# Kernel tuning notes

Measured on AMD Instinct MI355X. Metric: run time of the kernel, lower is better.

## Reference

```python
import jax, jax.numpy as jnp
import numpy as np

B, S, D, H = 2, 2048, 768, 12
DK = D // H
DF = 3072
SOFTCAP = 30.0
LN_EPS = 1e-5
NEG_INF = -1e30


def layer_norm(x, g, b):
    m = jnp.mean(x, axis=-1, keepdims=True)
    v = jnp.mean(jnp.square(x - m), axis=-1, keepdims=True)
    return (x - m) * jax.lax.rsqrt(v + LN_EPS) * g + b


def setup_inputs() -> dict:
    key = jax.random.key(0)
    ks = jax.random.split(key, 12)
    s = 0.02
    x = jax.random.normal(ks[0], (B, S, D), jnp.float32)
    count_bias = jax.random.normal(ks[1], (B, 1, S, S), jnp.float32)
    # causal mask: True = allowed
    attn_mask = jnp.broadcast_to(jnp.tril(jnp.ones((S, S), bool)), (B, 1, S, S))
    Wq = jax.random.normal(ks[2], (D, D), jnp.float32) * s
    Wk = jax.random.normal(ks[3], (D, D), jnp.float32) * s
    Wv = jax.random.normal(ks[4], (D, D), jnp.float32) * s
    Wo = jax.random.normal(ks[5], (D, D), jnp.float32) * s
    W1 = jax.random.normal(ks[6], (D, DF), jnp.float32) * s
    W2 = jax.random.normal(ks[7], (DF, D), jnp.float32) * s
    g1 = jnp.ones((D,), jnp.float32)
    b1 = jnp.zeros((D,), jnp.float32)
    g2 = jnp.ones((D,), jnp.float32)
    b2 = jnp.zeros((D,), jnp.float32)
    return dict(x=x, count_bias=count_bias, attn_mask=attn_mask, Wq=Wq, Wk=Wk,
                Wv=Wv, Wo=Wo, W1=W1, W2=W2, g1=g1, b1=b1, g2=g2, b2=b2)


def reference(x, count_bias, attn_mask, Wq, Wk, Wv, Wo, W1, W2, g1, b1, g2, b2):
    # pre-norm (note: residual taken from normed activations, faithful to source)
    h = layer_norm(x, g1, b1)                                   # (B,S,D)
    q = (h @ Wq).reshape(B, S, H, DK).transpose(0, 2, 1, 3)     # (B,H,S,DK)
    k = (h @ Wk).reshape(B, S, H, DK).transpose(0, 2, 1, 3)
    v = (h @ Wv).reshape(B, S, H, DK).transpose(0, 2, 1, 3)
    scale = 1.0 / np.sqrt(DK).astype(np.float32)
    scores = jnp.einsum('bhqd,bhkd->bhqk', q, k) * scale + count_bias
    scores = jnp.tanh(scores / SOFTCAP) * SOFTCAP               # softcap
    scores = jnp.where(attn_mask, scores, NEG_INF)
    weights = jax.nn.softmax(scores, axis=-1)
    o = jnp.einsum('bhqk,bhkd->bhqd', weights, v)               # (B,H,S,DK)
    o = o.transpose(0, 2, 1, 3).reshape(B, S, D) @ Wo
    x1 = o + h
    h2 = layer_norm(x1, g2, b2)
    ffn = jax.nn.gelu(h2 @ W1, approximate=False) @ W2
    return ffn + h2
```

## Files before the change

### kernel.cpp

```cpp
#include <hip/hip_runtime.h>
#include <hip/hip_bf16.h>
#include <cstdint>

#define Bn 2
#define Sn 2048
#define Dn 768
#define Hn 12
#define DKn 64
#define DFn 3072
#define Mrows 4096

typedef float f32x4 __attribute__((ext_vector_type(4)));
typedef __bf16 bf16x8 __attribute__((ext_vector_type(8)));
typedef short s16x8 __attribute__((ext_vector_type(8)));
typedef short s16x4 __attribute__((ext_vector_type(4)));

__device__ __forceinline__ f32x4 MFMA(s16x8 a, s16x8 b, f32x4 c) {
  return __builtin_amdgcn_mfma_f32_16x16x32_bf16(
      __builtin_bit_cast(bf16x8, a), __builtin_bit_cast(bf16x8, b), c, 0, 0, 0);
}

__device__ __forceinline__ void g2lds16(const void* g, void* l) {
  __builtin_amdgcn_global_load_lds(
      (__attribute__((address_space(1))) void*)(g),
      (__attribute__((address_space(3))) void*)(l), 16, 0, 0);
}

__device__ __forceinline__ short f2bf(float f) {
  unsigned u = __builtin_bit_cast(unsigned, f);
  unsigned r = (u + 0x7fffu + ((u >> 16) & 1u)) >> 16;
  return (short)r;
}

__global__ void wtrans(const float* __restrict__ in, short* __restrict__ out, int R, int C) {
  __shared__ float t[32][33];
  int c0 = blockIdx.x * 32, r0 = blockIdx.y * 32;
  int tx = threadIdx.x, ty = threadIdx.y;
#pragma unroll
  for (int i = 0; i < 4; i++) t[ty + i * 8][tx] = in[(size_t)(r0 + ty + i * 8) * C + c0 + tx];
  __syncthreads();
#pragma unroll
  for (int i = 0; i < 4; i++) out[(size_t)(c0 + ty + i * 8) * R + r0 + tx] = f2bf(t[tx][ty + i * 8]);
}

__global__ __launch_bounds__(256) void ln_kernel(const float* __restrict__ x,
                                                 const float* __restrict__ g,
                                                 const float* __restrict__ b,
                                                 short* __restrict__ hb,
                                                 float* __restrict__ hf) {
  int row = blockIdx.x;
  const float* xr = x + (size_t)row * Dn;
  int tid = threadIdx.x;
  float v[3];
  float s = 0.f, ss = 0.f;
#pragma unroll
  for (int i = 0; i < 3; i++) {
    v[i] = xr[tid + i * 256];
    s += v[i];
    ss += v[i] * v[i];
  }
#pragma unroll
  for (int m = 1; m < 64; m <<= 1) {
    s += __shfl_xor(s, m);
    ss += __shfl_xor(ss, m);
  }
  __shared__ float red[8];
  int w = tid >> 6, lane = tid & 63;
  if (lane == 0) { red[w] = s; red[4 + w] = ss; }
  __syncthreads();
  s = red[0] + red[1] + red[2] + red[3];
  ss = red[4] + red[5] + red[6] + red[7];
  float mean = s * (1.0f / Dn);
  float var = ss * (1.0f / Dn) - mean * mean;
  float rs = rsqrtf(var + 1e-5f);
#pragma unroll
  for (int i = 0; i < 3; i++) {
    int c = tid + i * 256;
    float h = (v[i] - mean) * rs * g[c] + b[c];
    hb[(size_t)row * Dn + c] = f2bf(h);
    hf[(size_t)row * Dn + c] = h;
  }
}

template <int EPI>
__global__ __launch_bounds__(256) void gemm_bt(const short* __restrict__ A,
                                               const short* __restrict__ Bt,
                                               short* __restrict__ Cb,
                                               const float* __restrict__ addm,
                                               float* __restrict__ Cf,
                                               int M, int N, int K) {
  __shared__ __align__(16) short As[4096];
  __shared__ __align__(16) short Bs[4096];
  int tid = threadIdx.x;
  int lane = tid & 63, w = tid >> 6, g = lane >> 4, lt = lane & 15;
  int wr = w >> 1, wc = w & 1;
  int m0 = blockIdx.x * 128, n0 = blockIdx.y * 128;
  int sr = tid >> 2, su = (tid & 3) * 8;
  const short* Ag = A + (size_t)(m0 + sr) * K + su;
  const short* Bg = Bt + (size_t)(n0 + sr) * K + su;
  f32x4 acc[4][4] = {};
  for (int k0 = 0; k0 < K; k0 += 32) {
    g2lds16(Ag + k0, &As[tid * 8]);
    g2lds16(Ag + k0 + (size_t)64 * K, &As[2048 + tid * 8]);
    g2lds16(Bg + k0, &Bs[tid * 8]);
    g2lds16(Bg + k0 + (size_t)64 * K, &Bs[2048 + tid * 8]);
    __syncthreads();
    s16x8 af[4], bfr[4];
#pragma unroll
    for (int i = 0; i < 4; i++) {
      af[i] = *(const s16x8*)&As[(wr * 64 + i * 16 + lt) * 32 + g * 8];
      bfr[i] = *(const s16x8*)&Bs[(wc * 64 + i * 16 + lt) * 32 + g * 8];
    }
#pragma unroll
    for (int mi = 0; mi < 4; mi++)
#pragma unroll
      for (int ni = 0; ni < 4; ni++) acc[mi][ni] = MFMA(af[mi], bfr[ni], acc[mi][ni]);
    __syncthreads();
  }
#pragma unroll
  for (int mi = 0; mi < 4; mi++) {
    int m = m0 + wr * 64 + mi * 16 + g * 4;
#pragma unroll
    for (int ni = 0; ni < 4; ni++) {
      int n = n0 + wc * 64 + ni * 16 + lt;
#pragma unroll
      for (int r = 0; r < 4; r++) {
        float v = acc[mi][ni][r];
        size_t idx = (size_t)(m + r) * N + n;
        if constexpr (EPI == 0) {
          Cb[idx] = f2bf(v);
        } else if constexpr (EPI == 1) {
          float ge = 0.5f * v * (1.0f + erff(v * 0.70710678f));
          Cb[idx] = f2bf(ge);
        } else {
          Cf[idx] = v + addm[idx];
        }
      }
    }
  }
}

__global__ void vtrans(const short* __restrict__ qkv, short* __restrict__ vt) {
  __shared__ short t[32][33];
  int bh = blockIdx.z;
  int b = bh / Hn, h = bh % Hn;
  int s0 = blockIdx.x * 32, d0 = blockIdx.y * 32;
  int tx = threadIdx.x, ty = threadIdx.y;
#pragma unroll
  for (int i = 0; i < 4; i++)
    t[ty + i * 8][tx] =
        qkv[(size_t)(b * Sn + s0 + ty + i * 8) * (3 * Dn) + 2 * Dn + h * DKn + d0 + tx];
  __syncthreads();
#pragma unroll
  for (int i = 0; i < 4; i++)
    vt[(size_t)(bh * DKn + d0 + ty + i * 8) * Sn + s0 + tx] = t[tx][ty + i * 8];
}

__global__ __launch_bounds__(256) void attn_kernel(const short* __restrict__ qkv,
                                                   const short* __restrict__ vt,
                                                   const float* __restrict__ bias,
                                                   short* __restrict__ o) {
  __shared__ __align__(16) short plds[4][16][72];
  __shared__ __align__(16) float obuf[4][16][68];
  __shared__ float lsumbuf[4][16];
  int bh = blockIdx.x;
  int qt = 127 - (int)blockIdx.y;
  int b = bh / Hn, h = bh - b * Hn;
  int tid = threadIdx.x, w = tid >> 6, lane = tid & 63, g = lane >> 4, lt = lane & 15;
  int q0 = qt * 16;
  const short* qbase = qkv + (size_t)(b * Sn + q0 + lt) * (3 * Dn) + h * DKn;
  s16x8 qf0 = *(const s16x8*)(qbase + g * 8);
  s16x8 qf1 = *(const s16x8*)(qbase + 32 + g * 8);
  f32x4 oacc[4] = {};
  float lsum[4] = {0.f, 0.f, 0.f, 0.f};
  int n64 = (q0 + 16 + 63) >> 6;
  const float* biasrow = bias + ((size_t)b * Sn + q0 + g * 4) * Sn;
  const float C1 = 0.0120224586f;
  const float C2 = 0.0961796722f;
  const float C3 = -86.5617013f;
  for (int j = w; j < n64; j += 4) {
    int kc0 = j << 6;
    const short* kbase = qkv + (size_t)(b * Sn + kc0 + lt) * (3 * Dn) + Dn + h * DKn;
    s16x8 kf[4][2];
#pragma unroll
    for (int c = 0; c < 4; c++) {
      kf[c][0] = *(const s16x8*)(kbase + (size_t)c * 16 * (3 * Dn) + g * 8);
      kf[c][1] = *(const s16x8*)(kbase + (size_t)c * 16 * (3 * Dn) + 32 + g * 8);
    }
    float bb[4][4];
#pragma unroll
    for (int c = 0; c < 4; c++)
#pragma unroll
      for (int r = 0; r < 4; r++)
        bb[c][r] = biasrow[(size_t)r * Sn + kc0 + c * 16 + lt] * C2;
    f32x4 s[4] = {};
#pragma unroll
    for (int c = 0; c < 4; c++) {
      s[c] = MFMA(qf0, kf[c][0], s[c]);
      s[c] = MFMA(qf1, kf[c][1], s[c]);
    }
    const short* vbase = vt + ((size_t)bh * DKn + lt) * Sn + kc0 + g * 8;
    s16x8 vf[4][2];
#pragma unroll
    for (int dt = 0; dt < 4; dt++) {
      vf[dt][0] = *(const s16x8*)(vbase + (size_t)dt * 16 * Sn);
      vf[dt][1] = *(const s16x8*)(vbase + (size_t)dt * 16 * Sn + 32);
    }
    bool needmask = (kc0 + 63 > q0);
#pragma unroll
    for (int c = 0; c < 4; c++) {
#pragma unroll
      for (int r = 0; r < 4; r++) {
        float targ = fmaf(s[c][r], C1, bb[c][r]);
        float t = __builtin_amdgcn_exp2f(targ);
        float u = __builtin_amdgcn_rcpf(1.0f + t);
        float p = __builtin_amdgcn_exp2f(C3 * u);
        if (needmask) p = (kc0 + c * 16 + lt <= q0 + g * 4 + r) ? p : 0.0f;
        lsum[r] += p;
        plds[w][g * 4 + r][c * 16 + lt] = f2bf(p);
      }
    }
    s16x8 pf0 = *(const s16x8*)&plds[w][lt][g * 8];
    s16x8 pf1 = *(const s16x8*)&plds[w][lt][32 + g * 8];
#pragma unroll
    for (int dt = 0; dt < 4; dt++) {
      oacc[dt] = MFMA(pf0, vf[dt][0], oacc[dt]);
      oacc[dt] = MFMA(pf1, vf[dt][1], oacc[dt]);
    }
  }
#pragma unroll
  for (int r = 0; r < 4; r++) {
    float l = lsum[r];
    l += __shfl_xor(l, 1);
    l += __shfl_xor(l, 2);
    l += __shfl_xor(l, 4);
    l += __shfl_xor(l, 8);
    lsum[r] = l;
  }
#pragma unroll
  for (int dt = 0; dt < 4; dt++)
#pragma unroll
    for (int r = 0; r < 4; r++) obuf[w][g * 4 + r][dt * 16 + lt] = oacc[dt][r];
  if (lt == 0) {
#pragma unroll
    for (int r = 0; r < 4; r++) lsumbuf[w][g * 4 + r] = lsum[r];
  }
  __syncthreads();
  int q = tid >> 4, dk0 = (tid & 15) * 4;
  f32x4 a0 = *(const f32x4*)&obuf[0][q][dk0];
  f32x4 a1 = *(const f32x4*)&obuf[1][q][dk0];
  f32x4 a2 = *(const f32x4*)&obuf[2][q][dk0];
  f32x4 a3 = *(const f32x4*)&obuf[3][q][dk0];
  float l = lsumbuf[0][q] + lsumbuf[1][q] + lsumbuf[2][q] + lsumbuf[3][q];
  float inv = __builtin_amdgcn_rcpf(l);
  f32x4 acc = (a0 + a1) + (a2 + a3);
  s16x4 outv;
  outv[0] = f2bf(acc[0] * inv);
  outv[1] = f2bf(acc[1] * inv);
  outv[2] = f2bf(acc[2] * inv);
  outv[3] = f2bf(acc[3] * inv);
  *(s16x4*)&o[(size_t)(b * Sn + q0 + q) * Dn + h * DKn + dk0] = outv;
}

extern "C" void kernel_launch(void* const* d_in, const int* in_sizes, int n_in,
                              void* d_out, int out_size, void* d_ws, size_t ws_size,
                              hipStream_t stream) {
  const float* x = (const float*)d_in[0];
  const float* bias = (const float*)d_in[1];
  const float* Wq = (const float*)d_in[3];
  const float* Wk = (const float*)d_in[4];
  const float* Wv = (const float*)d_in[5];
  const float* Wo = (const float*)d_in[6];
  const float* W1 = (const float*)d_in[7];
  const float* W2 = (const float*)d_in[8];
  const float* g1 = (const float*)d_in[9];
  const float* b1 = (const float*)d_in[10];
  const float* g2 = (const float*)d_in[11];
  const float* b2 = (const float*)d_in[12];
  float* out = (float*)d_out;
  char* ws = (char*)d_ws;

  short* wqkv_t = (short*)(ws + 0);
  short* wo_t = (short*)(ws + 3538944);
  short* w1_t = (short*)(ws + 4718592);
  short* w2_t = (short*)(ws + 9437184);
  short* hb = (short*)(ws + 14155776);
  float* hf = (float*)(ws + 20447232);
  short* qkv = (short*)(ws + 33030144);
  short* a1 = qkv;
  short* vt = (short*)(ws + 58195968);
  float* x1 = (float*)(ws + 58195968);
  short* o_ = (short*)(ws + 70778880);
  short* h2b = hb;
  float* h2f = hf;

  dim3 tb(32, 8);
  wtrans<<<dim3(24, 24), tb, 0, stream>>>(Wq, wqkv_t, Dn, Dn);
  wtrans<<<dim3(24, 24), tb, 0, stream>>>(Wk, wqkv_t + (size_t)Dn * Dn, Dn, Dn);
  wtrans<<<dim3(24, 24), tb, 0, stream>>>(Wv, wqkv_t + (size_t)2 * Dn * Dn, Dn, Dn);
  wtrans<<<dim3(24, 24), tb, 0, stream>>>(Wo, wo_t, Dn, Dn);
  wtrans<<<dim3(96, 24), tb, 0, stream>>>(W1, w1_t, Dn, DFn);
  wtrans<<<dim3(24, 96), tb, 0, stream>>>(W2, w2_t, DFn, Dn);

  ln_kernel<<<Mrows, 256, 0, stream>>>(x, g1, b1, hb, hf);

  gemm_bt<0><<<dim3(32, 18), 256, 0, stream>>>(hb, wqkv_t, qkv, nullptr, nullptr,
                                               Mrows, 3 * Dn, Dn);
  vtrans<<<dim3(64, 2, Bn * Hn), tb, 0, stream>>>(qkv, vt);
  attn_kernel<<<dim3(24, 128), 256, 0, stream>>>(qkv, vt, bias, o_);

  gemm_bt<2><<<dim3(32, 6), 256, 0, stream>>>(o_, wo_t, nullptr, hf, x1,
                                              Mrows, Dn, Dn);
  ln_kernel<<<Mrows, 256, 0, stream>>>(x1, g2, b2, h2b, h2f);
  gemm_bt<1><<<dim3(32, 24), 256, 0, stream>>>(h2b, w1_t, a1, nullptr, nullptr,
                                               Mrows, DFn, Dn);
  gemm_bt<2><<<dim3(32, 6), 256, 0, stream>>>(a1, w2_t, nullptr, h2f, out,
                                              Mrows, Dn, DFn);
}
```

Before: 418.8 us.

## Share K/V tiles across waves via LDS in attention; add 64x64 GEMM for narrow outputs

Attention now assigns 64 query rows per block, one 16-row slice per wave. K and V tiles are staged once into double-buffered, swizzled LDS through async global-to-LDS loads and shared by all four waves, replacing per-wave direct global loads and the cross-wave reduction. Query tiles are interleaved from both ends of the causal range to balance work across blocks. A new 64x64-tile GEMM is used for the N=768 projections (Wo and W2) to launch more blocks and fill the GPU better, at the cost of less operand reuse per block.

```diff
diff --git a/kernel.cpp b/kernel.cpp
--- a/kernel.cpp
+++ b/kernel.cpp
@@ -140,6 +140,84 @@
   }
 }
 
+template <int EPI>
+__global__ __launch_bounds__(256, 4) void gemm64(const short* __restrict__ A,
+                                                 const short* __restrict__ Bt,
+                                                 short* __restrict__ Cb,
+                                                 const float* __restrict__ addm,
+                                                 float* __restrict__ Cf,
+                                                 int M, int N, int K) {
+  __shared__ __align__(16) short As[2][4096];
+  __shared__ __align__(16) short Bs[2][4096];
+  int tid = threadIdx.x, lane = tid & 63, w = tid >> 6, g = lane >> 4, lt = lane & 15;
+  int wr = w >> 1, wc = w & 1;
+  int m0 = blockIdx.x * 64, n0 = blockIdx.y * 64;
+  int r0 = tid >> 3, cc = (tid & 7) ^ (r0 & 7);
+  const short* asrc0 = A + (size_t)(m0 + r0) * K + cc * 8;
+  const short* asrc1 = A + (size_t)(m0 + r0 + 32) * K + cc * 8;
+  const short* bsrc0 = Bt + (size_t)(n0 + r0) * K + cc * 8;
+  const short* bsrc1 = Bt + (size_t)(n0 + r0 + 32) * K + cc * 8;
+  int sw = lt & 7;
+  int ch0 = (g ^ sw) * 8, ch1 = ((4 + g) ^ sw) * 8;
+  f32x4 acc[2][2] = {};
+  g2lds16(asrc0, &As[0][tid * 8]);
+  g2lds16(asrc1, &As[0][2048 + tid * 8]);
+  g2lds16(bsrc0, &Bs[0][tid * 8]);
+  g2lds16(bsrc1, &Bs[0][2048 + tid * 8]);
+  __syncthreads();
+  int nsteps = K >> 6;
+  for (int t = 0; t < nsteps; t++) {
+    int cur = t & 1;
+    if (t + 1 < nsteps) {
+      int k0 = (t + 1) << 6;
+      g2lds16(asrc0 + k0, &As[cur ^ 1][tid * 8]);
+      g2lds16(asrc1 + k0, &As[cur ^ 1][2048 + tid * 8]);
+      g2lds16(bsrc0 + k0, &Bs[cur ^ 1][tid * 8]);
+      g2lds16(bsrc1 + k0, &Bs[cur ^ 1][2048 + tid * 8]);
+    }
+    s16x8 af[2][2], bf[2][2];
+#pragma unroll
+    for (int mi = 0; mi < 2; mi++) {
+      af[mi][0] = *(const s16x8*)&As[cur][(wr * 32 + mi * 16 + lt) * 64 + ch0];
+      af[mi][1] = *(const s16x8*)&As[cur][(wr * 32 + mi * 16 + lt) * 64 + ch1];
+    }
+#pragma unroll
+    for (int ni = 0; ni < 2; ni++) {
+      bf[ni][0] = *(const s16x8*)&Bs[cur][(wc * 32 + ni * 16 + lt) * 64 + ch0];
+      bf[ni][1] = *(const s16x8*)&Bs[cur][(wc * 32 + ni * 16 + lt) * 64 + ch1];
+    }
+#pragma unroll
+    for (int mi = 0; mi < 2; mi++)
+#pragma unroll
+      for (int ni = 0; ni < 2; ni++) {
+        acc[mi][ni] = MFMA(af[mi][0], bf[ni][0], acc[mi][ni]);
+        acc[mi][ni] = MFMA(af[mi][1], bf[ni][1], acc[mi][ni]);
+      }
+    __syncthreads();
+  }
+#pragma unroll
+  for (int mi = 0; mi < 2; mi++) {
+    int m = m0 + wr * 32 + mi * 16 + g * 4;
+#pragma unroll
+    for (int ni = 0; ni < 2; ni++) {
+      int n = n0 + wc * 32 + ni * 16 + lt;
+#pragma unroll
+      for (int r = 0; r < 4; r++) {
+        float v = acc[mi][ni][r];
+        size_t idx = (size_t)(m + r) * N + n;
+        if constexpr (EPI == 0) {
+          Cb[idx] = f2bf(v);
+        } else if constexpr (EPI == 1) {
+          float ge = 0.5f * v * (1.0f + erff(v * 0.70710678f));
+          Cb[idx] = f2bf(ge);
+        } else {
+          Cf[idx] = v + addm[idx];
+        }
+      }
+    }
+  }
+}
+
 __global__ void vtrans(const short* __restrict__ qkv, short* __restrict__ vt) {
   __shared__ short t[32][33];
   int bh = blockIdx.z;
@@ -156,36 +234,51 @@
     vt[(size_t)(bh * DKn + d0 + ty + i * 8) * Sn + s0 + tx] = t[tx][ty + i * 8];
 }
 
-__global__ __launch_bounds__(256) void attn_kernel(const short* __restrict__ qkv,
-                                                   const short* __restrict__ vt,
-                                                   const float* __restrict__ bias,
-                                                   short* __restrict__ o) {
+__global__ __launch_bounds__(256, 3) void attn_kernel(const short* __restrict__ qkv,
+                                                      const short* __restrict__ vt,
+                                                      const float* __restrict__ bias,
+                                                      short* __restrict__ o) {
+  __shared__ __align__(16) short Ks[2][4096];
+  __shared__ __align__(16) short Vs[2][4096];
   __shared__ __align__(16) short plds[4][16][72];
-  __shared__ __align__(16) float obuf[4][16][68];
-  __shared__ float lsumbuf[4][16];
   int bh = blockIdx.x;
-  int qt = 127 - (int)blockIdx.y;
+  int by = blockIdx.y;
+  int qt = (by & 1) ? (31 - (by >> 1)) : (by >> 1);
   int b = bh / Hn, h = bh - b * Hn;
   int tid = threadIdx.x, w = tid >> 6, lane = tid & 63, g = lane >> 4, lt = lane & 15;
-  int q0 = qt * 16;
+  int q0 = qt * 64 + w * 16;
   const short* qbase = qkv + (size_t)(b * Sn + q0 + lt) * (3 * Dn) + h * DKn;
   s16x8 qf0 = *(const s16x8*)(qbase + g * 8);
   s16x8 qf1 = *(const s16x8*)(qbase + 32 + g * 8);
-  f32x4 oacc[4] = {};
-  float lsum[4] = {0.f, 0.f, 0.f, 0.f};
-  int n64 = (q0 + 16 + 63) >> 6;
+  int sr0 = tid >> 3, scc = (tid & 7) ^ (sr0 & 7);
+  const short* kseg = qkv + (size_t)b * Sn * (3 * Dn) + Dn + h * DKn;
+  const short* ksrc0 = kseg + (size_t)sr0 * (3 * Dn) + scc * 8;
+  const short* ksrc1 = kseg + (size_t)(sr0 + 32) * (3 * Dn) + scc * 8;
+  const short* vseg = vt + (size_t)bh * DKn * Sn;
+  const short* vsrc0 = vseg + (size_t)sr0 * Sn + scc * 8;
+  const short* vsrc1 = vseg + (size_t)(sr0 + 32) * Sn + scc * 8;
+  int sw = lt & 7;
+  int ch0 = (g ^ sw) * 8, ch1 = ((4 + g) ^ sw) * 8;
   const float* biasrow = bias + ((size_t)b * Sn + q0 + g * 4) * Sn;
   const float C1 = 0.0120224586f;
   const float C2 = 0.0961796722f;
   const float C3 = -86.5617013f;
-  for (int j = w; j < n64; j += 4) {
-    int kc0 = j << 6;
-    const short* kbase = qkv + (size_t)(b * Sn + kc0 + lt) * (3 * Dn) + Dn + h * DKn;
-    s16x8 kf[4][2];
-#pragma unroll
-    for (int c = 0; c < 4; c++) {
-      kf[c][0] = *(const s16x8*)(kbase + (size_t)c * 16 * (3 * Dn) + g * 8);
-      kf[c][1] = *(const s16x8*)(kbase + (size_t)c * 16 * (3 * Dn) + 32 + g * 8);
+  f32x4 oacc[4] = {};
+  float lsum[4] = {0.f, 0.f, 0.f, 0.f};
+  g2lds16(ksrc0, &Ks[0][tid * 8]);
+  g2lds16(ksrc1, &Ks[0][2048 + tid * 8]);
+  g2lds16(vsrc0, &Vs[0][tid * 8]);
+  g2lds16(vsrc1, &Vs[0][2048 + tid * 8]);
+  __syncthreads();
+  for (int t = 0; t <= qt; t++) {
+    int cur = t & 1;
+    int kc0 = t * 64;
+    if (t < qt) {
+      size_t koff = (size_t)(kc0 + 64) * (3 * Dn);
+      g2lds16(ksrc0 + koff, &Ks[cur ^ 1][tid * 8]);
+      g2lds16(ksrc1 + koff, &Ks[cur ^ 1][2048 + tid * 8]);
+      g2lds16(vsrc0 + kc0 + 64, &Vs[cur ^ 1][tid * 8]);
+      g2lds16(vsrc1 + kc0 + 64, &Vs[cur ^ 1][2048 + tid * 8]);
     }
     float bb[4][4];
 #pragma unroll
@@ -193,27 +286,32 @@
 #pragma unroll
       for (int r = 0; r < 4; r++)
         bb[c][r] = biasrow[(size_t)r * Sn + kc0 + c * 16 + lt] * C2;
+    s16x8 kf[4][2];
+#pragma unroll
+    for (int c = 0; c < 4; c++) {
+      kf[c][0] = *(const s16x8*)&Ks[cur][(c * 16 + lt) * 64 + ch0];
+      kf[c][1] = *(const s16x8*)&Ks[cur][(c * 16 + lt) * 64 + ch1];
+    }
     f32x4 s[4] = {};
 #pragma unroll
     for (int c = 0; c < 4; c++) {
       s[c] = MFMA(qf0, kf[c][0], s[c]);
       s[c] = MFMA(qf1, kf[c][1], s[c]);
     }
-    const short* vbase = vt + ((size_t)bh * DKn + lt) * Sn + kc0 + g * 8;
     s16x8 vf[4][2];
 #pragma unroll
     for (int dt = 0; dt < 4; dt++) {
-      vf[dt][0] = *(const s16x8*)(vbase + (size_t)dt * 16 * Sn);
-      vf[dt][1] = *(const s16x8*)(vbase + (size_t)dt * 16 * Sn + 32);
-    }
-    bool needmask = (kc0 + 63 > q0);
+      vf[dt][0] = *(const s16x8*)&Vs[cur][(dt * 16 + lt) * 64 + ch0];
+      vf[dt][1] = *(const s16x8*)&Vs[cur][(dt * 16 + lt) * 64 + ch1];
+    }
+    bool needmask = (t == qt);
 #pragma unroll
     for (int c = 0; c < 4; c++) {
 #pragma unroll
       for (int r = 0; r < 4; r++) {
         float targ = fmaf(s[c][r], C1, bb[c][r]);
-        float t = __builtin_amdgcn_exp2f(targ);
-        float u = __builtin_amdgcn_rcpf(1.0f + t);
+        float e = __builtin_amdgcn_exp2f(targ);
+        float u = __builtin_amdgcn_rcpf(1.0f + e);
         float p = __builtin_amdgcn_exp2f(C3 * u);
         if (needmask) p = (kc0 + c * 16 + lt <= q0 + g * 4 + r) ? p : 0.0f;
         lsum[r] += p;
@@ -227,7 +325,9 @@
       oacc[dt] = MFMA(pf0, vf[dt][0], oacc[dt]);
       oacc[dt] = MFMA(pf1, vf[dt][1], oacc[dt]);
     }
-  }
+    __syncthreads();
+  }
+  float inv[4];
 #pragma unroll
   for (int r = 0; r < 4; r++) {
     float l = lsum[r];
@@ -235,31 +335,13 @@
     l += __shfl_xor(l, 2);
     l += __shfl_xor(l, 4);
     l += __shfl_xor(l, 8);
-    lsum[r] = l;
-  }
+    inv[r] = __builtin_amdgcn_rcpf(l);
+  }
+  short* obase = o + (size_t)(b * Sn + q0 + g * 4) * Dn + h * DKn + lt;
 #pragma unroll
   for (int dt = 0; dt < 4; dt++)
 #pragma unroll
-    for (int r = 0; r < 4; r++) obuf[w][g * 4 + r][dt * 16 + lt] = oacc[dt][r];
-  if (lt == 0) {
-#pragma unroll
-    for (int r = 0; r < 4; r++) lsumbuf[w][g * 4 + r] = lsum[r];
-  }
-  __syncthreads();
-  int q = tid >> 4, dk0 = (tid & 15) * 4;
-  f32x4 a0 = *(const f32x4*)&obuf[0][q][dk0];
-  f32x4 a1 = *(const f32x4*)&obuf[1][q][dk0];
-  f32x4 a2 = *(const f32x4*)&obuf[2][q][dk0];
-  f32x4 a3 = *(const f32x4*)&obuf[3][q][dk0];
-  float l = lsumbuf[0][q] + lsumbuf[1][q] + lsumbuf[2][q] + lsumbuf[3][q];
-  float inv = __builtin_amdgcn_rcpf(l);
-  f32x4 acc = (a0 + a1) + (a2 + a3);
-  s16x4 outv;
-  outv[0] = f2bf(acc[0] * inv);
-  outv[1] = f2bf(acc[1] * inv);
-  outv[2] = f2bf(acc[2] * inv);
-  outv[3] = f2bf(acc[3] * inv);
-  *(s16x4*)&o[(size_t)(b * Sn + q0 + q) * Dn + h * DKn + dk0] = outv;
+    for (int r = 0; r < 4; r++) obase[(size_t)r * Dn + dt * 16] = f2bf(oacc[dt][r] * inv[r]);
 }
 
 extern "C" void kernel_launch(void* const* d_in, const int* in_sizes, int n_in,
@@ -307,13 +389,13 @@
   gemm_bt<0><<<dim3(32, 18), 256, 0, stream>>>(hb, wqkv_t, qkv, nullptr, nullptr,
                                                Mrows, 3 * Dn, Dn);
   vtrans<<<dim3(64, 2, Bn * Hn), tb, 0, stream>>>(qkv, vt);
-  attn_kernel<<<dim3(24, 128), 256, 0, stream>>>(qkv, vt, bias, o_);
-
-  gemm_bt<2><<<dim3(32, 6), 256, 0, stream>>>(o_, wo_t, nullptr, hf, x1,
+  attn_kernel<<<dim3(24, 32), 256, 0, stream>>>(qkv, vt, bias, o_);
+
+  gemm64<2><<<dim3(64, 12), 256, 0, stream>>>(o_, wo_t, nullptr, hf, x1,
                                               Mrows, Dn, Dn);
   ln_kernel<<<Mrows, 256, 0, stream>>>(x1, g2, b2, h2b, h2f);
   gemm_bt<1><<<dim3(32, 24), 256, 0, stream>>>(h2b, w1_t, a1, nullptr, nullptr,
                                                Mrows, DFn, Dn);
-  gemm_bt<2><<<dim3(32, 6), 256, 0, stream>>>(a1, w2_t, nullptr, h2f, out,
+  gemm64<2><<<dim3(64, 12), 256, 0, stream>>>(a1, w2_t, nullptr, h2f, out,
                                               Mrows, Dn, DFn);
 }
```

After: 335.1 us. 1.25x faster.
